# Performance work log

Measured on AMD Instinct MI355X. Metric: run time of the kernel, lower is better.

## Reference

```python
import jax, jax.numpy as jnp
import numpy as np

EPS = 1e-9


def _approx_match(xyz1, xyz2):
    """Faithful reimplementation of Fan et al. approxmatch CUDA kernel.

    xyz1: (b, n, 3), xyz2: (b, m, 3)
    Returns (match (b,n,m), sqdist (b,n,m)).
    """
    b, n, _ = xyz1.shape
    m = xyz2.shape[1]
    # pairwise squared distances (b, n, m)
    d2 = jnp.sum((xyz1[:, :, None, :] - xyz2[:, None, :, :]) ** 2, axis=-1)
    mx = float(max(n, m))
    remainL = jnp.full((b, n), mx / n, dtype=xyz1.dtype)  # mass left on xyz1 side
    remainR = jnp.full((b, m), mx / m, dtype=xyz1.dtype)  # mass left on xyz2 side
    match = jnp.zeros((b, n, m), dtype=xyz1.dtype)
    # annealing schedule: level = -4^j for j = 7..-1, then level = 0
    for j in range(7, -3, -1):
        level = 0.0 if j == -2 else -(4.0 ** j)
        w = jnp.exp(level * d2) * remainR[:, None, :]                    # (b,n,m)
        w = w / (jnp.sum(w, axis=2, keepdims=True) + EPS) * remainL[:, :, None]
        sumr = jnp.sum(w, axis=1)                                        # (b,m)
        cons = jnp.minimum(remainR / (sumr + EPS), 1.0)                  # column saturation
        w = w * cons[:, None, :]
        match = match + w
        remainL = jnp.maximum(remainL - jnp.sum(w, axis=2), 0.0)
        remainR = jnp.maximum(remainR - sumr * cons, 0.0)
    return match, d2


def setup_inputs() -> dict:
    key = jax.random.key(0)
    k1, k2 = jax.random.split(key)
    xyz1 = jax.random.normal(k1, (16, 2048, 3), dtype=jnp.float32)
    xyz2 = jax.random.normal(k2, (16, 2048, 3), dtype=jnp.float32)
    return {"xyz1": xyz1, "xyz2": xyz2}


def reference(xyz1, xyz2):
    # matchcost_forward: cost_b = sum_{i,l} match[i,l] * ||x1_i - x2_l||
    match, d2 = _approx_match(xyz1, xyz2)
    return jnp.sum(match * jnp.sqrt(d2), axis=(1, 2))  # (b,)
```

## Files before the change

### kernel.cpp

```cpp
#include <hip/hip_runtime.h>

#define BB 16
#define NN 2048
#define MM 2048
#define EPSF 1e-9f
#define SKIPT (-135.0f)

typedef float v2f __attribute__((ext_vector_type(2)));

constexpr int CH = 64;

__global__ __launch_bounds__(256) void init_kernel(
    const float* __restrict__ xyz1, const float* __restrict__ xyz2,
    float4* __restrict__ P1, float4* __restrict__ P2,
    float* __restrict__ remR0,
    float* __restrict__ stRS, float* __restrict__ stU,
    float* __restrict__ stS, float* __restrict__ stT,
    float* __restrict__ out)
{
    const int t = blockIdx.x * 256 + threadIdx.x;
    if (t < BB * NN) {
        P1[t] = make_float4(xyz1[3*t+0], xyz1[3*t+1], xyz1[3*t+2], 0.0f);
        stRS[t] = 0.0f; stRS[BB*NN + t] = 0.0f;
        stU[t]  = 0.0f; stU[BB*NN + t]  = 0.0f;
    }
    if (t < BB * MM) {
        P2[t] = make_float4(xyz2[3*t+0], xyz2[3*t+1], xyz2[3*t+2], 0.0f);
        remR0[t] = 1.0f;
        stS[t] = 0.0f; stS[BB*MM + t] = 0.0f;
        stT[t] = 0.0f; stT[BB*MM + t] = 0.0f;
    }
    if (t < BB) out[t] = 0.0f;
}

__global__ __launch_bounds__(256) void rowInit(
    const float4* __restrict__ P1, const float4* __restrict__ P2,
    float* __restrict__ stRSacc, float coef)
{
    __shared__ float4 sCol[CH];
    const int chunks = MM / CH;
    const int bpb = (NN / 512) * chunks;
    const int batch = blockIdx.x / bpb;
    const int rem   = blockIdx.x % bpb;
    const int rg    = rem / chunks;
    const int ic    = rem % chunks;
    const int t     = threadIdx.x;

    if (t < CH) sCol[t] = P2[batch * MM + ic * CH + t];
    __syncthreads();

    const int row0 = batch * NN + rg * 512 + t;
    const int row1 = row0 + 256;
    const float4 p0 = P1[row0];
    const float4 p1 = P1[row1];
    const v2f px = {p0.x, p1.x}, py = {p0.y, p1.y}, pz = {p0.z, p1.z};
    v2f rs = {0.0f, 0.0f};
#pragma unroll 4
    for (int ii = 0; ii < CH; ++ii) {
        const float4 q = sCol[ii];
        const v2f dx = px - q.x, dy = py - q.y, dz = pz - q.z;
        const v2f g = coef * (dx*dx + dy*dy + dz*dz);
        if (__ballot((g.x > SKIPT) || (g.y > SKIPT))) {
            v2f e;
            e.x = __builtin_amdgcn_exp2f(g.x);
            e.y = __builtin_amdgcn_exp2f(g.y);
            rs += e;
        }
    }
    atomicAdd(&stRSacc[row0], rs.x);
    atomicAdd(&stRSacc[row1], rs.y);
}

template<int MODE, bool SPARSE>
__global__ __launch_bounds__(256) void colK(
    const float4* __restrict__ P1, const float4* __restrict__ P2,
    const float* __restrict__ stRSr, const float* __restrict__ stUr,
    float* __restrict__ stRSz, float* __restrict__ stUz,
    const float* __restrict__ remLr, float* __restrict__ remLw,
    const float* __restrict__ scaler, float* __restrict__ scalew,
    float* __restrict__ stS, float* __restrict__ stT,
    float coef)
{
    __shared__ float4 sRow[CH];
    const int chunks = NN / CH;
    const int bpb = (MM / 512) * chunks;
    const int batch = blockIdx.x / bpb;
    const int rem   = blockIdx.x % bpb;
    const int cg    = rem / chunks;
    const int ic    = rem % chunks;
    const int t     = threadIdx.x;

    if (t < CH) {
        const int gi = batch * NN + ic * CH + t;
        float L;
        if (MODE == 0) L = 1.0f;
        else           L = fmaxf(remLr[gi] - scaler[gi] * stUr[gi], 0.0f);
        remLw[gi] = L;
        const float sc = L / (stRSr[gi] + EPSF);
        scalew[gi] = sc;
        const float4 p = P1[gi];
        sRow[t] = make_float4(p.x, p.y, p.z, sc);
        stRSz[gi] = 0.0f; stUz[gi] = 0.0f;
    }
    __syncthreads();

    const int col0 = batch * MM + cg * 512 + t;
    const int col1 = col0 + 256;
    const float4 q0 = P2[col0];
    const float4 q1 = P2[col1];
    const v2f qx = {q0.x, q1.x}, qy = {q0.y, q1.y}, qz = {q0.z, q1.z};
    v2f s = {0.0f, 0.0f}, tt = {0.0f, 0.0f};
#pragma unroll 4
    for (int ii = 0; ii < CH; ++ii) {
        const float4 a = sRow[ii];
        const v2f dx = a.x - qx, dy = a.y - qy, dz = a.z - qz;
        const v2f d2 = dx*dx + dy*dy + dz*dz;
        if (SPARSE) {
            const v2f g = coef * d2;
            if (__ballot((g.x > SKIPT) || (g.y > SKIPT))) {
                v2f e;
                e.x = __builtin_amdgcn_exp2f(g.x);
                e.y = __builtin_amdgcn_exp2f(g.y);
                e *= a.w;
                v2f sq;
                sq.x = __builtin_amdgcn_sqrtf(d2.x);
                sq.y = __builtin_amdgcn_sqrtf(d2.y);
                s += e;
                tt += e * sq;
            }
        } else {
            v2f e;
            if (MODE == 2) { e.x = a.w; e.y = a.w; }
            else {
                const v2f g = coef * d2;
                e.x = a.w * __builtin_amdgcn_exp2f(g.x);
                e.y = a.w * __builtin_amdgcn_exp2f(g.y);
            }
            v2f sq;
            sq.x = __builtin_amdgcn_sqrtf(d2.x);
            sq.y = __builtin_amdgcn_sqrtf(d2.y);
            s += e;
            tt += e * sq;
        }
    }
    atomicAdd(&stS[col0], s.x);
    atomicAdd(&stT[col0], tt.x);
    atomicAdd(&stS[col1], s.y);
    atomicAdd(&stT[col1], tt.y);
}

template<int MODE, bool SPARSE>
__global__ __launch_bounds__(256) void rowK(
    const float4* __restrict__ P1, const float4* __restrict__ P2,
    const float* __restrict__ stSr, const float* __restrict__ stTr,
    float* __restrict__ stSz, float* __restrict__ stTz,
    const float* __restrict__ remRr, float* __restrict__ remRw,
    float* __restrict__ stRS, float* __restrict__ stU,
    float* __restrict__ out,
    float coefP, float coefN)
{
    __shared__ float4 sCol[CH];
    __shared__ float  sPc[CH];
    const int chunks = MM / CH;
    const int bpb = (NN / 512) * chunks;
    const int batch = blockIdx.x / bpb;
    const int rem   = blockIdx.x % bpb;
    const int rg    = rem / chunks;
    const int ic    = rem % chunks;
    const int t     = threadIdx.x;

    float c = 0.0f;
    if (t < CH) {
        const int gl = batch * MM + ic * CH + t;
        const float R  = remRr[gl];
        const float s  = stSr[gl];
        const float t2 = stTr[gl];
        const float sumr = s * R;
        const float cons = fminf(R / (sumr + EPSF), 1.0f);
        const float pcol = R * cons;
        const float Rn   = fmaxf(R - sumr * cons, 0.0f);
        remRw[gl] = Rn;
        const float4 p = P2[gl];
        sCol[t] = make_float4(p.x, p.y, p.z, Rn);
        sPc[t]  = pcol;
        stSz[gl] = 0.0f; stTz[gl] = 0.0f;
        if (rg == 0) c = pcol * t2;
    }
    if (rg == 0) {
#pragma unroll
        for (int off = 32; off > 0; off >>= 1) c += __shfl_xor(c, off, 64);
        if (t < CH && (t & 63) == 0) atomicAdd(out + batch, c);
    }
    __syncthreads();

    const int row0 = batch * NN + rg * 512 + t;
    const int row1 = row0 + 256;
    const float4 p0 = P1[row0];
    const float4 p1 = P1[row1];
    const v2f px = {p0.x, p1.x}, py = {p0.y, p1.y}, pz = {p0.z, p1.z};
    v2f rs = {0.0f, 0.0f}, u = {0.0f, 0.0f};
#pragma unroll 4
    for (int ii = 0; ii < CH; ++ii) {
        const float4 q = sCol[ii];
        const float pc = sPc[ii];
        const v2f dx = px - q.x, dy = py - q.y, dz = pz - q.z;
        const v2f d2 = dx*dx + dy*dy + dz*dz;
        if (MODE == 1) {
            const v2f g = coefN * d2;
            if (SPARSE) {
                if (__ballot((g.x > SKIPT) || (g.y > SKIPT))) {
                    v2f en;
                    en.x = __builtin_amdgcn_exp2f(g.x);
                    en.y = __builtin_amdgcn_exp2f(g.y);
                    const v2f e2 = en * en;
                    const v2f e4 = e2 * e2;
                    u  += e4 * pc;
                    rs += en * q.w;
                }
            } else {
                v2f en;
                en.x = __builtin_amdgcn_exp2f(g.x);
                en.y = __builtin_amdgcn_exp2f(g.y);
                const v2f e2 = en * en;
                const v2f e4 = e2 * e2;
                u  += e4 * pc;
                rs += en * q.w;
            }
        } else {
            const v2f g = coefP * d2;
            v2f ep;
            ep.x = __builtin_amdgcn_exp2f(g.x);
            ep.y = __builtin_amdgcn_exp2f(g.y);
            u  += ep * pc;
            rs += q.w;
        }
    }
    atomicAdd(&stRS[row0], rs.x);
    atomicAdd(&stU[row0], u.x);
    atomicAdd(&stRS[row1], rs.y);
    atomicAdd(&stU[row1], u.y);
}

__global__ __launch_bounds__(256) void finCost(
    const float* __restrict__ stSr, const float* __restrict__ stTr,
    const float* __restrict__ remRr, float* __restrict__ out)
{
    const int idx = blockIdx.x * 256 + threadIdx.x;
    const int batch = idx / MM;
    const float R = remRr[idx];
    const float sumr = stSr[idx] * R;
    const float cons = fminf(R / (sumr + EPSF), 1.0f);
    float c = R * cons * stTr[idx];
#pragma unroll
    for (int off = 32; off > 0; off >>= 1) c += __shfl_xor(c, off, 64);
    if ((threadIdx.x & 63) == 0) atomicAdd(out + batch, c);
}

extern "C" void kernel_launch(void* const* d_in, const int* in_sizes, int n_in,
                              void* d_out, int out_size, void* d_ws, size_t ws_size,
                              hipStream_t stream)
{
    const float* xyz1 = (const float*)d_in[0];
    const float* xyz2 = (const float*)d_in[1];
    float* out = (float*)d_out;

    const int BN = BB * NN, BM = BB * MM;
    float4* P1 = (float4*)d_ws;
    float4* P2 = P1 + BN;
    float* remL  = (float*)(P2 + BM);
    float* scale = remL + 2 * BN;
    float* remR  = scale + 2 * BN;
    float* stRS  = remR + 2 * BM;
    float* stU   = stRS + 2 * BN;
    float* stS   = stU + 2 * BN;
    float* stT   = stS + 2 * BM;

    init_kernel<<<dim3(BN / 256), dim3(256), 0, stream>>>(
        xyz1, xyz2, P1, P2, remR, stRS, stU, stS, stT, out);

    float coef[10];
    const double lv[10] = {-16384.0, -4096.0, -1024.0, -256.0, -64.0,
                           -16.0, -4.0, -1.0, -0.25, 0.0};
    for (int i = 0; i < 10; ++i) coef[i] = (float)(lv[i] * 1.4426950408889634);

    dim3 grid(BB * 4 * (NN / CH));
    dim3 fgrid(BM / 256);
    dim3 blk(256);

    rowInit<<<grid, blk, 0, stream>>>(P1, P2, stRS + 1 * BN, coef[0]);

    for (int j = 0; j < 10; ++j) {
        const int p = j & 1, q = 1 - p;
        if (j == 0)
            colK<0, true><<<grid, blk, 0, stream>>>(P1, P2,
                stRS + q*BN, stU + q*BN, stRS + p*BN, stU + p*BN,
                remL + p*BN, remL + q*BN, scale + p*BN, scale + q*BN,
                stS + p*BM, stT + p*BM, coef[0]);
        else if (j <= 3)
            colK<1, true><<<grid, blk, 0, stream>>>(P1, P2,
                stRS + q*BN, stU + q*BN, stRS + p*BN, stU + p*BN,
                remL + p*BN, remL + q*BN, scale + p*BN, scale + q*BN,
                stS + p*BM, stT + p*BM, coef[j]);
        else if (j == 9)
            colK<2, false><<<grid, blk, 0, stream>>>(P1, P2,
                stRS + q*BN, stU + q*BN, stRS + p*BN, stU + p*BN,
                remL + p*BN, remL + q*BN, scale + p*BN, scale + q*BN,
                stS + p*BM, stT + p*BM, coef[9]);
        else
            colK<1, false><<<grid, blk, 0, stream>>>(P1, P2,
                stRS + q*BN, stU + q*BN, stRS + p*BN, stU + p*BN,
                remL + p*BN, remL + q*BN, scale + p*BN, scale + q*BN,
                stS + p*BM, stT + p*BM, coef[j]);

        if (j < 9) {
            if (j <= 2)
                rowK<1, true><<<grid, blk, 0, stream>>>(P1, P2,
                    stS + p*BM, stT + p*BM, stS + q*BM, stT + q*BM,
                    remR + p*BM, remR + q*BM,
                    stRS + p*BN, stU + p*BN, out, coef[j], coef[j+1]);
            else if (j < 8)
                rowK<1, false><<<grid, blk, 0, stream>>>(P1, P2,
                    stS + p*BM, stT + p*BM, stS + q*BM, stT + q*BM,
                    remR + p*BM, remR + q*BM,
                    stRS + p*BN, stU + p*BN, out, coef[j], coef[j+1]);
            else
                rowK<2, false><<<grid, blk, 0, stream>>>(P1, P2,
                    stS + p*BM, stT + p*BM, stS + q*BM, stT + q*BM,
                    remR + p*BM, remR + q*BM,
                    stRS + p*BN, stU + p*BN, out, coef[8], 0.0f);
        }
    }
    finCost<<<fgrid, blk, 0, stream>>>(stS + 1*BM, stT + 1*BM, remR + 1*BM, out);
}
```

Before: 509.5 us.

## Replace atomic accumulation with per-chunk partial buffers reduced by consumers

Each row/column kernel now writes its per-chunk partial sums into a separate slice (32 chunks) instead of atomically adding into shared accumulators. The consuming kernel sums the 32 partials in a block-level two-stage reduction before use, and the zeroing of accumulators is removed. This trades atomic contention and the zeroing stores for extra global reads of 32x larger partial buffers on every stage.

Measured after the change: 550.1 us. 8.0% more time.

```diff
diff --git a/kernel.cpp b/kernel.cpp
--- a/kernel.cpp
+++ b/kernel.cpp
@@ -9,33 +9,26 @@
 typedef float v2f __attribute__((ext_vector_type(2)));
 
 constexpr int CH = 64;
+constexpr int NCHUNK = 32;
 
 __global__ __launch_bounds__(256) void init_kernel(
     const float* __restrict__ xyz1, const float* __restrict__ xyz2,
     float4* __restrict__ P1, float4* __restrict__ P2,
-    float* __restrict__ remR0,
-    float* __restrict__ stRS, float* __restrict__ stU,
-    float* __restrict__ stS, float* __restrict__ stT,
-    float* __restrict__ out)
+    float* __restrict__ remR0, float* __restrict__ out)
 {
     const int t = blockIdx.x * 256 + threadIdx.x;
-    if (t < BB * NN) {
+    if (t < BB * NN)
         P1[t] = make_float4(xyz1[3*t+0], xyz1[3*t+1], xyz1[3*t+2], 0.0f);
-        stRS[t] = 0.0f; stRS[BB*NN + t] = 0.0f;
-        stU[t]  = 0.0f; stU[BB*NN + t]  = 0.0f;
-    }
     if (t < BB * MM) {
         P2[t] = make_float4(xyz2[3*t+0], xyz2[3*t+1], xyz2[3*t+2], 0.0f);
         remR0[t] = 1.0f;
-        stS[t] = 0.0f; stS[BB*MM + t] = 0.0f;
-        stT[t] = 0.0f; stT[BB*MM + t] = 0.0f;
     }
     if (t < BB) out[t] = 0.0f;
 }
 
 __global__ __launch_bounds__(256) void rowInit(
     const float4* __restrict__ P1, const float4* __restrict__ P2,
-    float* __restrict__ stRSacc, float coef)
+    float* __restrict__ RSp, float coef)
 {
     __shared__ float4 sCol[CH];
     const int chunks = MM / CH;
@@ -67,21 +60,22 @@
             rs += e;
         }
     }
-    atomicAdd(&stRSacc[row0], rs.x);
-    atomicAdd(&stRSacc[row1], rs.y);
+    float* dst = RSp + ic * (BB * NN);
+    dst[row0] = rs.x;
+    dst[row1] = rs.y;
 }
 
 template<int MODE, bool SPARSE>
 __global__ __launch_bounds__(256) void colK(
     const float4* __restrict__ P1, const float4* __restrict__ P2,
-    const float* __restrict__ stRSr, const float* __restrict__ stUr,
-    float* __restrict__ stRSz, float* __restrict__ stUz,
+    const float* __restrict__ RSp, const float* __restrict__ Up,
     const float* __restrict__ remLr, float* __restrict__ remLw,
     const float* __restrict__ scaler, float* __restrict__ scalew,
-    float* __restrict__ stS, float* __restrict__ stT,
+    float* __restrict__ Sp, float* __restrict__ Tp,
     float coef)
 {
     __shared__ float4 sRow[CH];
+    __shared__ float redA[256], redB[256];
     const int chunks = NN / CH;
     const int bpb = (MM / 512) * chunks;
     const int batch = blockIdx.x / bpb;
@@ -90,17 +84,34 @@
     const int ic    = rem % chunks;
     const int t     = threadIdx.x;
 
+    {
+        const int r = t & 63, g4 = t >> 6;
+        const int gi = batch * NN + ic * CH + r;
+        float aRS = 0.0f, aU = 0.0f;
+#pragma unroll
+        for (int k = 0; k < 8; ++k) {
+            const int c = g4 * 8 + k;
+            aRS += RSp[c * (BB*NN) + gi];
+            if (MODE != 0) aU += Up[c * (BB*NN) + gi];
+        }
+        redA[t] = aRS;
+        redB[t] = aU;
+    }
+    __syncthreads();
     if (t < CH) {
         const int gi = batch * NN + ic * CH + t;
+        const float rsum = redA[t] + redA[t+64] + redA[t+128] + redA[t+192];
         float L;
         if (MODE == 0) L = 1.0f;
-        else           L = fmaxf(remLr[gi] - scaler[gi] * stUr[gi], 0.0f);
+        else {
+            const float usum = redB[t] + redB[t+64] + redB[t+128] + redB[t+192];
+            L = fmaxf(remLr[gi] - scaler[gi] * usum, 0.0f);
+        }
         remLw[gi] = L;
-        const float sc = L / (stRSr[gi] + EPSF);
+        const float sc = L / (rsum + EPSF);
         scalew[gi] = sc;
         const float4 p = P1[gi];
         sRow[t] = make_float4(p.x, p.y, p.z, sc);
-        stRSz[gi] = 0.0f; stUz[gi] = 0.0f;
     }
     __syncthreads();
 
@@ -143,24 +154,24 @@
             tt += e * sq;
         }
     }
-    atomicAdd(&stS[col0], s.x);
-    atomicAdd(&stT[col0], tt.x);
-    atomicAdd(&stS[col1], s.y);
-    atomicAdd(&stT[col1], tt.y);
+    float* dS = Sp + ic * (BB*MM);
+    float* dT = Tp + ic * (BB*MM);
+    dS[col0] = s.x;  dT[col0] = tt.x;
+    dS[col1] = s.y;  dT[col1] = tt.y;
 }
 
 template<int MODE, bool SPARSE>
 __global__ __launch_bounds__(256) void rowK(
     const float4* __restrict__ P1, const float4* __restrict__ P2,
-    const float* __restrict__ stSr, const float* __restrict__ stTr,
-    float* __restrict__ stSz, float* __restrict__ stTz,
+    const float* __restrict__ Sp, const float* __restrict__ Tp,
     const float* __restrict__ remRr, float* __restrict__ remRw,
-    float* __restrict__ stRS, float* __restrict__ stU,
+    float* __restrict__ RSp, float* __restrict__ Up,
     float* __restrict__ out,
     float coefP, float coefN)
 {
     __shared__ float4 sCol[CH];
     __shared__ float  sPc[CH];
+    __shared__ float  redA[256], redB[256];
     const int chunks = MM / CH;
     const int bpb = (NN / 512) * chunks;
     const int batch = blockIdx.x / bpb;
@@ -169,12 +180,26 @@
     const int ic    = rem % chunks;
     const int t     = threadIdx.x;
 
-    float c = 0.0f;
+    {
+        const int r = t & 63, g4 = t >> 6;
+        const int gl = batch * MM + ic * CH + r;
+        float aS = 0.0f, aT = 0.0f;
+#pragma unroll
+        for (int k = 0; k < 8; ++k) {
+            const int c = g4 * 8 + k;
+            aS += Sp[c * (BB*MM) + gl];
+            aT += Tp[c * (BB*MM) + gl];
+        }
+        redA[t] = aS;
+        redB[t] = aT;
+    }
+    __syncthreads();
+    float cacc = 0.0f;
     if (t < CH) {
         const int gl = batch * MM + ic * CH + t;
+        const float s  = redA[t] + redA[t+64] + redA[t+128] + redA[t+192];
+        const float t2 = redB[t] + redB[t+64] + redB[t+128] + redB[t+192];
         const float R  = remRr[gl];
-        const float s  = stSr[gl];
-        const float t2 = stTr[gl];
         const float sumr = s * R;
         const float cons = fminf(R / (sumr + EPSF), 1.0f);
         const float pcol = R * cons;
@@ -183,13 +208,12 @@
         const float4 p = P2[gl];
         sCol[t] = make_float4(p.x, p.y, p.z, Rn);
         sPc[t]  = pcol;
-        stSz[gl] = 0.0f; stTz[gl] = 0.0f;
-        if (rg == 0) c = pcol * t2;
+        if (rg == 0) cacc = pcol * t2;
     }
     if (rg == 0) {
 #pragma unroll
-        for (int off = 32; off > 0; off >>= 1) c += __shfl_xor(c, off, 64);
-        if (t < CH && (t & 63) == 0) atomicAdd(out + batch, c);
+        for (int off = 32; off > 0; off >>= 1) cacc += __shfl_xor(cacc, off, 64);
+        if (t == 0) atomicAdd(out + batch, cacc);
     }
     __syncthreads();
 
@@ -235,22 +259,28 @@
             rs += q.w;
         }
     }
-    atomicAdd(&stRS[row0], rs.x);
-    atomicAdd(&stU[row0], u.x);
-    atomicAdd(&stRS[row1], rs.y);
-    atomicAdd(&stU[row1], u.y);
+    float* dRS = RSp + ic * (BB*NN);
+    float* dU  = Up  + ic * (BB*NN);
+    dRS[row0] = rs.x;  dU[row0] = u.x;
+    dRS[row1] = rs.y;  dU[row1] = u.y;
 }
 
 __global__ __launch_bounds__(256) void finCost(
-    const float* __restrict__ stSr, const float* __restrict__ stTr,
+    const float* __restrict__ Sp, const float* __restrict__ Tp,
     const float* __restrict__ remRr, float* __restrict__ out)
 {
     const int idx = blockIdx.x * 256 + threadIdx.x;
     const int batch = idx / MM;
+    float s = 0.0f, t2 = 0.0f;
+#pragma unroll 8
+    for (int c = 0; c < NCHUNK; ++c) {
+        s  += Sp[c * (BB*MM) + idx];
+        t2 += Tp[c * (BB*MM) + idx];
+    }
     const float R = remRr[idx];
-    const float sumr = stSr[idx] * R;
+    const float sumr = s * R;
     const float cons = fminf(R / (sumr + EPSF), 1.0f);
-    float c = R * cons * stTr[idx];
+    float c = R * cons * t2;
 #pragma unroll
     for (int off = 32; off > 0; off >>= 1) c += __shfl_xor(c, off, 64);
     if ((threadIdx.x & 63) == 0) atomicAdd(out + batch, c);
@@ -270,13 +300,13 @@
     float* remL  = (float*)(P2 + BM);
     float* scale = remL + 2 * BN;
     float* remR  = scale + 2 * BN;
-    float* stRS  = remR + 2 * BM;
-    float* stU   = stRS + 2 * BN;
-    float* stS   = stU + 2 * BN;
-    float* stT   = stS + 2 * BM;
+    float* RSp   = remR + 2 * BM;
+    float* Up    = RSp + NCHUNK * BN;
+    float* Sp    = Up  + NCHUNK * BN;
+    float* Tp    = Sp  + NCHUNK * BM;
 
     init_kernel<<<dim3(BN / 256), dim3(256), 0, stream>>>(
-        xyz1, xyz2, P1, P2, remR, stRS, stU, stS, stT, out);
+        xyz1, xyz2, P1, P2, remR, out);
 
     float coef[10];
     const double lv[10] = {-16384.0, -4096.0, -1024.0, -256.0, -64.0,
@@ -287,48 +317,38 @@
     dim3 fgrid(BM / 256);
     dim3 blk(256);
 
-    rowInit<<<grid, blk, 0, stream>>>(P1, P2, stRS + 1 * BN, coef[0]);
+    rowInit<<<grid, blk, 0, stream>>>(P1, P2, RSp, coef[0]);
 
     for (int j = 0; j < 10; ++j) {
         const int p = j & 1, q = 1 - p;
         if (j == 0)
-            colK<0, true><<<grid, blk, 0, stream>>>(P1, P2,
-                stRS + q*BN, stU + q*BN, stRS + p*BN, stU + p*BN,
+            colK<0, true><<<grid, blk, 0, stream>>>(P1, P2, RSp, Up,
                 remL + p*BN, remL + q*BN, scale + p*BN, scale + q*BN,
-                stS + p*BM, stT + p*BM, coef[0]);
+                Sp, Tp, coef[0]);
         else if (j <= 3)
-            colK<1, true><<<grid, blk, 0, stream>>>(P1, P2,
-                stRS + q*BN, stU + q*BN, stRS + p*BN, stU + p*BN,
+            colK<1, true><<<grid, blk, 0, stream>>>(P1, P2, RSp, Up,
                 remL + p*BN, remL + q*BN, scale + p*BN, scale + q*BN,
-                stS + p*BM, stT + p*BM, coef[j]);
+                Sp, Tp, coef[j]);
         else if (j == 9)
-            colK<2, false><<<grid, blk, 0, stream>>>(P1, P2,
-                stRS + q*BN, stU + q*BN, stRS + p*BN, stU + p*BN,
+            colK<2, false><<<grid, blk, 0, stream>>>(P1, P2, RSp, Up,
                 remL + p*BN, remL + q*BN, scale + p*BN, scale + q*BN,
-                stS + p*BM, stT + p*BM, coef[9]);
+                Sp, Tp, coef[9]);
         else
-            colK<1, false><<<grid, blk, 0, stream>>>(P1, P2,
-                stRS + q*BN, stU + q*BN, stRS + p*BN, stU + p*BN,
+            colK<1, false><<<grid, blk, 0, stream>>>(P1, P2, RSp, Up,
                 remL + p*BN, remL + q*BN, scale + p*BN, scale + q*BN,
-                stS + p*BM, stT + p*BM, coef[j]);
+                Sp, Tp, coef[j]);
 
         if (j < 9) {
             if (j <= 2)
-                rowK<1, true><<<grid, blk, 0, stream>>>(P1, P2,
-                    stS + p*BM, stT + p*BM, stS + q*BM, stT + q*BM,
-                    remR + p*BM, remR + q*BM,
-                    stRS + p*BN, stU + p*BN, out, coef[j], coef[j+1]);
+                rowK<1, true><<<grid, blk, 0, stream>>>(P1, P2, Sp, Tp,
+                    remR + p*BM, remR + q*BM, RSp, Up, out, coef[j], coef[j+1]);
             else if (j < 8)
-                rowK<1, false><<<grid, blk, 0, stream>>>(P1, P2,
-                    stS + p*BM, stT + p*BM, stS + q*BM, stT + q*BM,
-                    remR + p*BM, remR + q*BM,
-                    stRS + p*BN, stU + p*BN, out, coef[j], coef[j+1]);
+                rowK<1, false><<<grid, blk, 0, stream>>>(P1, P2, Sp, Tp,
+                    remR + p*BM, remR + q*BM, RSp, Up, out, coef[j], coef[j+1]);
             else
-                rowK<2, false><<<grid, blk, 0, stream>>>(P1, P2,
-                    stS + p*BM, stT + p*BM, stS + q*BM, stT + q*BM,
-                    remR + p*BM, remR + q*BM,
-                    stRS + p*BN, stU + p*BN, out, coef[8], 0.0f);
-        }
-    }
-    finCost<<<fgrid, blk, 0, stream>>>(stS + 1*BM, stT + 1*BM, remR + 1*BM, out);
-}
+                rowK<2, false><<<grid, blk, 0, stream>>>(P1, P2, Sp, Tp,
+                    remR + p*BM, remR + q*BM, RSp, Up, out, coef[8], 0.0f);
+        }
+    }
+    finCost<<<fgrid, blk, 0, stream>>>(Sp, Tp, remR + 1*BM, out);
+}
```
